# Kernel optimization log

Hardware: AMD Instinct MI355X
Metric: run time of the kernel (lower is better)

Reference implementation:

```python
import jax, jax.numpy as jnp
import numpy as np
from jax import lax

V, D = 100000, 300          # vocab, embedding dim (pretrained_embeds shape)
F, FS, K = 256, 3, 5        # nof_filters, filters_size, k_for_maxpool
B, NS, LS, LQ = 64, 50, 60, 32  # batch, n_sents per doc, sent len, question len


def setup_inputs() -> dict:
    key = jax.random.key(0)
    ks = jax.random.split(key, 8)
    sentences = jax.random.randint(ks[0], (B, NS, LS), 0, V)
    question = jax.random.randint(ks[1], (B, LQ), 0, V)
    target_sents = jax.random.randint(ks[2], (B, NS), 0, 2)
    target_docs = jax.random.randint(ks[3], (B,), 0, 2)
    embeds = jax.random.normal(ks[4], (V, D), dtype=jnp.float32)          # frozen pretrained table
    filters = jax.random.normal(ks[5], (F, 1, FS, D), dtype=jnp.float32)  # shared quest/sent conv filters
    W = jax.random.normal(ks[6], (6,), dtype=jnp.float32) * 0.4           # linear_per_q weight
    b = jax.random.normal(ks[7], (1,), dtype=jnp.float32) * 0.1           # linear_per_q bias
    return dict(sentences=sentences, question=question, target_sents=target_sents,
                target_docs=target_docs, embeds=embeds, filters=filters, W=W, b=b)


def _conv(x, filters):
    # x: [N,L,D], filters: [F,1,FS,D] -> [N,L,F]; matches F.conv2d(pad=(FS-1,0)) then slicing last L rows
    fs = filters.shape[2]
    L = x.shape[1]
    y = lax.conv_general_dilated(x[:, None, :, :], filters, (1, 1),
                                 ((fs - 1, fs - 1), (0, 0)),
                                 dimension_numbers=('NCHW', 'OIHW', 'NCHW'))  # [N,F,L+fs-1,1]
    return jnp.transpose(y[:, :, -L:, 0], (0, 2, 1))


def _cos(q, s):
    # q: [B,LQ,d], s: [B,NS,LS,d] -> [NS,B,LQ,LS] cosine similarity matrices
    num = jnp.einsum('bqd,bnld->nbql', q, s)
    qn = jnp.linalg.norm(q, axis=-1)                      # [B,LQ]
    sn = jnp.transpose(jnp.linalg.norm(s, axis=-1), (1, 0, 2))  # [NS,B,LS]
    return num / (qn[None, :, :, None] * sn[:, :, None, :])


def _pool(sim, k):
    # k-max pooling over the sentence-length axis -> stack [max, mean-of-top-k]
    top = lax.top_k(sim, k)[0]
    return jnp.stack([top[..., 0], jnp.mean(top, axis=-1)], axis=-1)


def _bce(p, t):
    eps = 1e-7
    p = jnp.clip(p, eps, 1.0 - eps)
    return -jnp.mean(t * jnp.log(p) + (1.0 - t) * jnp.log1p(-p))


def reference(sentences, question, target_sents, target_docs, embeds, filters, W, b):
    qe = embeds[question]                                 # [B,LQ,D]
    se = embeds[sentences]                                # [B,NS,LS,D]
    sim_ins = _cos(qe, se)                                # [NS,B,LQ,LS]
    sim_oh = (sim_ins >= 1.0 - 1e-5).astype(jnp.float32)  # exact-match channel (unmasked, as in original)
    qc = _conv(qe, filters)                               # [B,LQ,F]
    sc = _conv(se.reshape(B * NS, LS, D), filters).reshape(B, NS, LS, F)
    sim_sen = _cos(qc, sc)                                # [NS,B,LQ,LS]
    qmask = (question > 0).astype(jnp.float32)            # pad id = 0
    smask = (sentences > 0).astype(jnp.float32)
    m = qmask[None, :, :, None] * jnp.transpose(smask, (1, 0, 2))[:, :, None, :]
    feats = jnp.concatenate([_pool(sim_ins * m, K), _pool(sim_sen * m, K), _pool(sim_oh, K)], axis=-1)
    feats = jnp.transpose(feats, (1, 0, 2, 3))            # [B,NS,LQ,6]
    sent_out = jax.nn.sigmoid(feats @ W + b[0])           # [B,NS,LQ]
    sentence_relevance = jnp.mean(sent_out, axis=-1)      # [B,NS]
    document_emitions = jnp.max(sentence_relevance, axis=-1)  # [B]
    loss = (_bce(sentence_relevance, target_sents.astype(jnp.float32)) +
            _bce(document_emitions, target_docs.astype(jnp.float32))) / 2.0
    return loss, sentence_relevance, document_emitions
```

## Files before the change

### kernel.cpp

```cpp
#include <hip/hip_runtime.h>
#include <math.h>

#define VB  64
#define NSS 50
#define LSS 60
#define LQQ 32
#define DD  300
#define FF  256

#define SEST 312
#define SROWS 66
#define SCST 264
#define SIMST 66
#define KKC 29
#define KKI 10
#define KKS 8

typedef __attribute__((ext_vector_type(8))) short bfrag;
typedef __attribute__((ext_vector_type(4))) float ffrag;

__device__ __forceinline__ unsigned short f2bf(float v) {
    unsigned int x = __float_as_uint(v);
    x += 0x7fffu + ((x >> 16) & 1u);
    return (unsigned short)(x >> 16);
}
__device__ __forceinline__ float bf2f(unsigned short u) {
    return __uint_as_float(((unsigned int)u) << 16);
}

__global__ __launch_bounds__(256) void k_fprep(const float* __restrict__ filters,
                                               unsigned short* __restrict__ filt_frag) {
    int idx0 = (blockIdx.x * 256 + threadIdx.x) * 4;
    int j0 = idx0 & 7, ln = (idx0 >> 3) & 63, nt = (idx0 >> 9) & 15, kk = idx0 >> 13;
    int f = nt * 16 + (ln & 15);
    int k0 = kk * 32 + ((ln >> 4) << 3) + j0;
    int t = k0 / SEST, d0 = k0 - t * SEST;
    ushort4 h = {0, 0, 0, 0};
    if (t < 3 && d0 < DD) {
        float4 v = *(const float4*)(filters + f * 900 + t * DD + d0);
        h.x = f2bf(v.x); h.y = f2bf(v.y); h.z = f2bf(v.z); h.w = f2bf(v.w);
    }
    *(ushort4*)(filt_frag + idx0) = h;
}

__global__ __launch_bounds__(512) void k_qprep(const int* __restrict__ question,
                                               const float* __restrict__ embeds,
                                               const unsigned short* __restrict__ filt_frag,
                                               unsigned short* __restrict__ qe_frag,
                                               unsigned short* __restrict__ qc_frag,
                                               float* __restrict__ q_inv,
                                               float* __restrict__ qc_inv) {
    const int b = blockIdx.x, tid = threadIdx.x, lane = tid & 63, w = tid >> 6;
    const int quad = lane >> 4, m16 = lane & 15;
    __shared__ __align__(16) unsigned short qeb[34 * SEST];
    __shared__ __align__(16) unsigned short qcb[LQQ * SCST];
    const int* qrow = question + b * LQQ;
    {
        ushort4 z4 = {0, 0, 0, 0};
        for (int i = tid; i < 96; i += 512) {
            int r = i / 3, c = 300 + (i - r * 3) * 4;
            *(ushort4*)(qeb + r * SEST + c) = z4;
        }
        for (int i = tid; i < 156; i += 512) {
            int r = i / 78, c = (i - r * 78) * 4;
            *(ushort4*)(qeb + (LQQ + r) * SEST + c) = z4;
        }
    }
    for (int i = tid; i < LQQ * 75; i += 512) {
        int r = i / 75, c = (i - r * 75) * 4;
        float4 v = *(const float4*)(embeds + (size_t)qrow[r] * DD + c);
        ushort4 h;
        h.x = f2bf(v.x); h.y = f2bf(v.y); h.z = f2bf(v.z); h.w = f2bf(v.w);
        *(ushort4*)(qeb + r * SEST + c) = h;
    }
    __syncthreads();
    if (tid < 256) {
        int r = tid >> 3, part = tid & 7;
        float s = 0.f;
        #pragma unroll
        for (int it = 0; it < 5; ++it) {
            if (!(it == 4 && part == 7)) {
                int c = part * 8 + it * 64;
                uint4 u = *(const uint4*)(qeb + r * SEST + c);
                float a0 = bf2f((unsigned short)(u.x & 0xffff)), a1 = bf2f((unsigned short)(u.x >> 16));
                float a2 = bf2f((unsigned short)(u.y & 0xffff)), a3 = bf2f((unsigned short)(u.y >> 16));
                float a4 = bf2f((unsigned short)(u.z & 0xffff)), a5 = bf2f((unsigned short)(u.z >> 16));
                float a6 = bf2f((unsigned short)(u.w & 0xffff)), a7 = bf2f((unsigned short)(u.w >> 16));
                s += a0 * a0 + a1 * a1 + a2 * a2 + a3 * a3 + a4 * a4 + a5 * a5 + a6 * a6 + a7 * a7;
            }
        }
        s += __shfl_down(s, 4, 64);
        s += __shfl_down(s, 2, 64);
        s += __shfl_down(s, 1, 64);
        if (part == 0) q_inv[b * LQQ + r] = 1.f / sqrtf(s);
    }
    for (int i8 = tid; i8 < KKI * 2 * 64; i8 += 512) {
        int ln = i8 & 63, mt = (i8 >> 6) & 1, kk = i8 >> 7;
        int q = mt * 16 + (ln & 15);
        int k0 = kk * 32 + ((ln >> 4) << 3);
        uint4 v = {0, 0, 0, 0};
        if (k0 < SEST) v = *(const uint4*)(qeb + q * SEST + k0);
        *(uint4*)(qe_frag + (size_t)b * (KKI * 2 * 512) + (size_t)i8 * 8) = v;
    }
    const int mtq = w & 1, w4 = (w >> 1) * 4;
    ffrag acc[4];
    #pragma unroll
    for (int i = 0; i < 4; ++i) acc[i] = (ffrag)0.f;
    {
        const bfrag* fF = (const bfrag*)filt_frag;
        bfrag bb[4], nb[4];
        #pragma unroll
        for (int i = 0; i < 4; ++i) bb[i] = fF[(w4 + i) * 64 + lane];
        for (int kk = 0; kk < KKC; ++kk) {
            if (kk + 1 < KKC) {
                #pragma unroll
                for (int i = 0; i < 4; ++i) nb[i] = fF[((kk + 1) * 16 + w4 + i) * 64 + lane];
            }
            const int kb = kk * 32 + quad * 8;
            bfrag a0 = *(const bfrag*)(qeb + (mtq * 16 + m16) * SEST + kb);
            #pragma unroll
            for (int i = 0; i < 4; ++i)
                acc[i] = __builtin_amdgcn_mfma_f32_16x16x32_bf16(a0, bb[i], acc[i], 0, 0, 0);
            #pragma unroll
            for (int i = 0; i < 4; ++i) bb[i] = nb[i];
        }
    }
    #pragma unroll
    for (int i = 0; i < 4; ++i) {
        int f = (w4 + i) * 16 + m16;
        #pragma unroll
        for (int r = 0; r < 4; ++r) {
            int q = mtq * 16 + quad * 4 + r;
            qcb[q * SCST + f] = f2bf(acc[i][r]);
        }
    }
    __syncthreads();
    if (tid < 256) {
        int r = tid >> 3, part = tid & 7;
        float s = 0.f;
        #pragma unroll
        for (int it = 0; it < 4; ++it) {
            int c = part * 8 + it * 64;
            uint4 u = *(const uint4*)(qcb + r * SCST + c);
            float a0 = bf2f((unsigned short)(u.x & 0xffff)), a1 = bf2f((unsigned short)(u.x >> 16));
            float a2 = bf2f((unsigned short)(u.y & 0xffff)), a3 = bf2f((unsigned short)(u.y >> 16));
            float a4 = bf2f((unsigned short)(u.z & 0xffff)), a5 = bf2f((unsigned short)(u.z >> 16));
            float a6 = bf2f((unsigned short)(u.w & 0xffff)), a7 = bf2f((unsigned short)(u.w >> 16));
            s += a0 * a0 + a1 * a1 + a2 * a2 + a3 * a3 + a4 * a4 + a5 * a5 + a6 * a6 + a7 * a7;
        }
        s += __shfl_down(s, 4, 64);
        s += __shfl_down(s, 2, 64);
        s += __shfl_down(s, 1, 64);
        if (part == 0) qc_inv[b * LQQ + r] = 1.f / sqrtf(s);
    }
    for (int i8 = tid; i8 < KKS * 2 * 64; i8 += 512) {
        int ln = i8 & 63, mt = (i8 >> 6) & 1, kk = i8 >> 7;
        int q = mt * 16 + (ln & 15);
        int k0 = kk * 32 + ((ln >> 4) << 3);
        *(uint4*)(qc_frag + (size_t)b * (KKS * 2 * 512) + (size_t)i8 * 8) =
            *(const uint4*)(qcb + q * SCST + k0);
    }
}

#define CONV_STEP(KKV, BB0, BB1) do {                                              \
    const int kb_ = (KKV) * 32 + quad * 8;                                         \
    bfrag a0_ = *(const bfrag*)(seb + (m16) * SEST + kb_);                         \
    bfrag a1_ = *(const bfrag*)(seb + (16 + m16) * SEST + kb_);                    \
    bfrag a2_ = *(const bfrag*)(seb + (32 + m16) * SEST + kb_);                    \
    bfrag a3_ = *(const bfrag*)(seb + (48 + m16) * SEST + kb_);                    \
    __builtin_amdgcn_s_setprio(1);                                                 \
    acc[0][0] = __builtin_amdgcn_mfma_f32_16x16x32_bf16(a0_, BB0, acc[0][0], 0, 0, 0); \
    acc[0][1] = __builtin_amdgcn_mfma_f32_16x16x32_bf16(a0_, BB1, acc[0][1], 0, 0, 0); \
    acc[1][0] = __builtin_amdgcn_mfma_f32_16x16x32_bf16(a1_, BB0, acc[1][0], 0, 0, 0); \
    acc[1][1] = __builtin_amdgcn_mfma_f32_16x16x32_bf16(a1_, BB1, acc[1][1], 0, 0, 0); \
    acc[2][0] = __builtin_amdgcn_mfma_f32_16x16x32_bf16(a2_, BB0, acc[2][0], 0, 0, 0); \
    acc[2][1] = __builtin_amdgcn_mfma_f32_16x16x32_bf16(a2_, BB1, acc[2][1], 0, 0, 0); \
    acc[3][0] = __builtin_amdgcn_mfma_f32_16x16x32_bf16(a3_, BB0, acc[3][0], 0, 0, 0); \
    acc[3][1] = __builtin_amdgcn_mfma_f32_16x16x32_bf16(a3_, BB1, acc[3][1], 0, 0, 0); \
    __builtin_amdgcn_s_setprio(0);                                                 \
} while (0)

__global__ __launch_bounds__(512, 6) void k_sent(
    const int* __restrict__ sentences, const int* __restrict__ question,
    const float* __restrict__ embeds,
    const unsigned short* __restrict__ filt_frag,
    const unsigned short* __restrict__ qe_frag,
    const unsigned short* __restrict__ qc_frag,
    const float* __restrict__ q_inv, const float* __restrict__ qc_inv,
    const float* __restrict__ W6, const float* __restrict__ b1,
    float* __restrict__ d_out) {
    const int blk = blockIdx.x;
    const int b = blk / NSS, n = blk - b * NSS;
    const int tid = threadIdx.x, lane = tid & 63, w = tid >> 6;
    const int quad = lane >> 4, m16 = lane & 15;
    const int w2 = w * 2;

    __shared__ __align__(16) unsigned short seb[SROWS * SEST];
    __shared__ __align__(16) float sim[LQQ * SIMST];
    __shared__ float sinv[64], scninv[64];
    __shared__ int sid[64];
    __shared__ int qid[LQQ];
    __shared__ float qm[LQQ], qiv[LQQ], qciv[LQQ];
    __shared__ float featq[LQQ][4];
    __shared__ float pr[LQQ];
    unsigned short* scb = seb;

    const bfrag* fF = (const bfrag*)filt_frag;
    bfrag b0a = fF[(w2) * 64 + lane];
    bfrag b0b = fF[(w2 + 1) * 64 + lane];

    const int* srow = sentences + ((size_t)b * NSS + n) * LSS;
    if (tid < 64) sid[tid] = (tid < LSS) ? srow[tid] : 0;
    if (tid < LQQ) {
        int qi = question[b * LQQ + tid];
        qid[tid] = qi; qm[tid] = qi > 0 ? 1.f : 0.f;
        qiv[tid] = q_inv[b * LQQ + tid]; qciv[tid] = qc_inv[b * LQQ + tid];
    }
    {
        ushort4 z4 = {0, 0, 0, 0};
        for (int i = tid; i < 180; i += 512) {
            int r = i / 3, c = 300 + (i - r * 3) * 4;
            *(ushort4*)(seb + r * SEST + c) = z4;
        }
        for (int i = tid; i < 468; i += 512) {
            int r = i / 78, c = (i - r * 78) * 4;
            *(ushort4*)(seb + (60 + r) * SEST + c) = z4;
        }
    }
    for (int i = tid; i < LSS * 75; i += 512) {
        int r = i / 75, c = (i - r * 75) * 4;
        float4 v = *(const float4*)(embeds + (size_t)srow[r] * DD + c);
        ushort4 h;
        h.x = f2bf(v.x); h.y = f2bf(v.y); h.z = f2bf(v.z); h.w = f2bf(v.w);
        *(ushort4*)(seb + r * SEST + c) = h;
    }
    __syncthreads();
    if (tid < 480) {
        int r = tid >> 3, part = tid & 7;
        float s = 0.f;
        #pragma unroll
        for (int it = 0; it < 5; ++it) {
            if (!(it == 4 && part == 7)) {
                int c = part * 8 + it * 64;
                uint4 u = *(const uint4*)(seb + r * SEST + c);
                float a0 = bf2f((unsigned short)(u.x & 0xffff)), a1 = bf2f((unsigned short)(u.x >> 16));
                float a2 = bf2f((unsigned short)(u.y & 0xffff)), a3 = bf2f((unsigned short)(u.y >> 16));
                float a4 = bf2f((unsigned short)(u.z & 0xffff)), a5 = bf2f((unsigned short)(u.z >> 16));
                float a6 = bf2f((unsigned short)(u.w & 0xffff)), a7 = bf2f((unsigned short)(u.w >> 16));
                s += a0 * a0 + a1 * a1 + a2 * a2 + a3 * a3 + a4 * a4 + a5 * a5 + a6 * a6 + a7 * a7;
            }
        }
        s += __shfl_down(s, 4, 64);
        s += __shfl_down(s, 2, 64);
        s += __shfl_down(s, 1, 64);
        if (part == 0) sinv[r] = 1.f / sqrtf(s);
    }
    if (tid >= 480 && tid < 484) sinv[60 + tid - 480] = 0.f;
    __syncthreads();

    ffrag acc[4][2];
    #pragma unroll
    for (int mt = 0; mt < 4; ++mt)
        #pragma unroll
        for (int i = 0; i < 2; ++i) acc[mt][i] = (ffrag)0.f;
    {
        bfrag b1a, b1b;
        for (int kk = 0; kk + 2 <= KKC; kk += 2) {
            b1a = fF[((kk + 1) * 16 + w2) * 64 + lane];
            b1b = fF[((kk + 1) * 16 + w2 + 1) * 64 + lane];
            CONV_STEP(kk, b0a, b0b);
            if (kk + 2 < KKC) {
                b0a = fF[((kk + 2) * 16 + w2) * 64 + lane];
                b0b = fF[((kk + 2) * 16 + w2 + 1) * 64 + lane];
            }
            CONV_STEP(kk + 1, b1a, b1b);
        }
        CONV_STEP(KKC - 1, b0a, b0b);
    }
    {
        const int mt = w >> 2, nt = w & 3;
        const bfrag* qF = (const bfrag*)qe_frag + ((size_t)b * KKI * 2 + mt) * 64 + lane;
        const unsigned short* sebr = seb + (nt * 16 + m16) * SEST + quad * 8;
        ffrag c0 = (ffrag)0.f;
        bfrag aq0 = qF[0];
        for (int kk = 0; kk < KKI; kk += 2) {
            bfrag aq1 = qF[(kk + 1) * 128];
            bfrag bL0 = *(const bfrag*)(sebr + kk * 32);
            c0 = __builtin_amdgcn_mfma_f32_16x16x32_bf16(aq0, bL0, c0, 0, 0, 0);
            if (kk + 2 < KKI) aq0 = qF[(kk + 2) * 128];
            bfrag bL1 = *(const bfrag*)(sebr + (kk + 1) * 32);
            c0 = __builtin_amdgcn_mfma_f32_16x16x32_bf16(aq1, bL1, c0, 0, 0, 0);
        }
        const int l_ = nt * 16 + m16;
        const float sm = sinv[l_] * (sid[l_] > 0 ? 1.f : 0.f);
        #pragma unroll
        for (int r = 0; r < 4; ++r) {
            int q = mt * 16 + quad * 4 + r;
            sim[q * SIMST + l_] = c0[r] * (qiv[q] * qm[q]) * sm;
        }
    }
    __syncthreads();

    if (tid < 256) {
        ushort4 z4 = {0, 0, 0, 0};
        int r4 = 60 + (tid >> 6), c4 = (tid & 63) * 4;
        *(ushort4*)(scb + r4 * SCST + c4) = z4;
    }
    #pragma unroll
    for (int mt = 0; mt < 4; ++mt)
        #pragma unroll
        for (int i = 0; i < 2; ++i) {
            int f = (w2 + i) * 16 + m16;
            #pragma unroll
            for (int r = 0; r < 4; ++r) {
                int l = mt * 16 + quad * 4 + r;
                scb[l * SCST + f] = f2bf(acc[mt][i][r]);
            }
        }
    if (tid < LQQ) {
        int q = tid;
        float t0 = -1e30f, t1 = -1e30f, t2 = -1e30f, t3 = -1e30f, t4 = -1e30f;
        for (int l = 0; l < LSS; ++l) {
            float v = sim[q * SIMST + l];
            if (v > t4) {
                if (v > t0)      { t4 = t3; t3 = t2; t2 = t1; t1 = t0; t0 = v; }
                else if (v > t1) { t4 = t3; t3 = t2; t2 = t1; t1 = v; }
                else if (v > t2) { t4 = t3; t3 = t2; t2 = v; }
                else if (v > t3) { t4 = t3; t3 = v; }
                else               t4 = v;
            }
        }
        featq[q][0] = t0;
        featq[q][1] = (t0 + t1 + t2 + t3 + t4) * 0.2f;
        int qi = qid[q], c = 0;
        for (int l = 0; l < LSS; ++l) c += (sid[l] == qi) ? 1 : 0;
        featq[q][2] = c > 0 ? 1.f : 0.f;
        featq[q][3] = (float)(c < 5 ? c : 5) * 0.2f;
    }
    __syncthreads();
    if (tid < 480) {
        int r = tid >> 3, part = tid & 7;
        float s = 0.f;
        #pragma unroll
        for (int it = 0; it < 4; ++it) {
            int c = part * 8 + it * 64;
            uint4 u = *(const uint4*)(scb + r * SCST + c);
            float a0 = bf2f((unsigned short)(u.x & 0xffff)), a1 = bf2f((unsigned short)(u.x >> 16));
            float a2 = bf2f((unsigned short)(u.y & 0xffff)), a3 = bf2f((unsigned short)(u.y >> 16));
            float a4 = bf2f((unsigned short)(u.z & 0xffff)), a5 = bf2f((unsigned short)(u.z >> 16));
            float a6 = bf2f((unsigned short)(u.w & 0xffff)), a7 = bf2f((unsigned short)(u.w >> 16));
            s += a0 * a0 + a1 * a1 + a2 * a2 + a3 * a3 + a4 * a4 + a5 * a5 + a6 * a6 + a7 * a7;
        }
        s += __shfl_down(s, 4, 64);
        s += __shfl_down(s, 2, 64);
        s += __shfl_down(s, 1, 64);
        if (part == 0) scninv[r] = 1.f / sqrtf(s);
    }
    if (tid >= 480 && tid < 484) scninv[60 + tid - 480] = 0.f;
    __syncthreads();
    {
        const int mt = w >> 2, nt = w & 3;
        const bfrag* qF = (const bfrag*)qc_frag + ((size_t)b * KKS * 2 + mt) * 64 + lane;
        const unsigned short* scbr = scb + (nt * 16 + m16) * SCST + quad * 8;
        ffrag c0 = (ffrag)0.f;
        bfrag aq0 = qF[0];
        for (int kk = 0; kk < KKS; kk += 2) {
            bfrag aq1 = qF[(kk + 1) * 128];
            bfrag bL0 = *(const bfrag*)(scbr + kk * 32);
            c0 = __builtin_amdgcn_mfma_f32_16x16x32_bf16(aq0, bL0, c0, 0, 0, 0);
            if (kk + 2 < KKS) aq0 = qF[(kk + 2) * 128];
            bfrag bL1 = *(const bfrag*)(scbr + (kk + 1) * 32);
            c0 = __builtin_amdgcn_mfma_f32_16x16x32_bf16(aq1, bL1, c0, 0, 0, 0);
        }
        const int l_ = nt * 16 + m16;
        const float sm = scninv[l_] * (sid[l_] > 0 ? 1.f : 0.f);
        #pragma unroll
        for (int r = 0; r < 4; ++r) {
            int q = mt * 16 + quad * 4 + r;
            sim[q * SIMST + l_] = c0[r] * (qciv[q] * qm[q]) * sm;
        }
    }
    __syncthreads();
    if (tid < LQQ) {
        int q = tid;
        float t0 = -1e30f, t1 = -1e30f, t2 = -1e30f, t3 = -1e30f, t4 = -1e30f;
        for (int l = 0; l < LSS; ++l) {
            float v = sim[q * SIMST + l];
            if (v > t4) {
                if (v > t0)      { t4 = t3; t3 = t2; t2 = t1; t1 = t0; t0 = v; }
                else if (v > t1) { t4 = t3; t3 = t2; t2 = t1; t1 = v; }
                else if (v > t2) { t4 = t3; t3 = t2; t2 = v; }
                else if (v > t3) { t4 = t3; t3 = v; }
                else               t4 = v;
            }
        }
        float smax = t0, smean = (t0 + t1 + t2 + t3 + t4) * 0.2f;
        float z = featq[q][0] * W6[0] + featq[q][1] * W6[1] + smax * W6[2] + smean * W6[3]
                + featq[q][2] * W6[4] + featq[q][3] * W6[5] + b1[0];
        pr[q] = 1.f / (1.f + expf(-z));
    }
    __syncthreads();
    if (w == 0) {
        float s = (lane < LQQ) ? pr[lane] : 0.f;
        s += __shfl_down(s, 16, 64);
        s += __shfl_down(s, 8, 64);
        s += __shfl_down(s, 4, 64);
        s += __shfl_down(s, 2, 64);
        s += __shfl_down(s, 1, 64);
        if (lane == 0) d_out[1 + (size_t)b * NSS + n] = s * (1.f / 32.f);
    }
}

__global__ __launch_bounds__(256) void k_final(const int* __restrict__ tsent,
                                               const int* __restrict__ tdoc,
                                               float* __restrict__ d_out) {
    const int tid = threadIdx.x;
    __shared__ float sh[256];
    __shared__ float docs[VB];
    if (tid < VB) {
        float m = -1e30f;
        for (int nn = 0; nn < NSS; ++nn) m = fmaxf(m, d_out[1 + tid * NSS + nn]);
        docs[tid] = m;
        d_out[1 + VB * NSS + tid] = m;
    }
    float s = 0.f;
    for (int i = tid; i < VB * NSS; i += 256) {
        float p = d_out[1 + i];
        p = fminf(fmaxf(p, 1e-7f), 1.f - 1e-7f);
        float t = (float)tsent[i];
        s += t * logf(p) + (1.f - t) * log1pf(-p);
    }
    sh[tid] = s;
    __syncthreads();
    for (int st = 128; st > 0; st >>= 1) {
        if (tid < st) sh[tid] += sh[tid + st];
        __syncthreads();
    }
    float ls = 0.f;
    if (tid == 0) ls = -sh[0] / (float)(VB * NSS);
    __syncthreads();
    float s2 = 0.f;
    if (tid < VB) {
        float p = fminf(fmaxf(docs[tid], 1e-7f), 1.f - 1e-7f);
        float t = (float)tdoc[tid];
        s2 = t * logf(p) + (1.f - t) * log1pf(-p);
    }
    sh[tid] = s2;
    __syncthreads();
    for (int st = 128; st > 0; st >>= 1) {
        if (tid < st) sh[tid] += sh[tid + st];
        __syncthreads();
    }
    if (tid == 0) {
        float ld = -sh[0] / (float)VB;
        d_out[0] = 0.5f * (ls + ld);
    }
}

extern "C" void kernel_launch(void* const* d_in, const int* in_sizes, int n_in,
                              void* d_out, int out_size, void* d_ws, size_t ws_size,
                              hipStream_t stream) {
    const int*   sentences = (const int*)d_in[0];
    const int*   question  = (const int*)d_in[1];
    const int*   tsent     = (const int*)d_in[2];
    const int*   tdoc      = (const int*)d_in[3];
    const float* embeds    = (const float*)d_in[4];
    const float* filters   = (const float*)d_in[5];
    const float* W6        = (const float*)d_in[6];
    const float* b1        = (const float*)d_in[7];
    float* out = (float*)d_out;

    float* ws = (float*)d_ws;
    float* q_inv  = ws;
    float* qc_inv = ws + 2048;
    unsigned short* qe_frag  = (unsigned short*)(ws + 4096);
    unsigned short* qc_frag  = qe_frag + 655360;
    unsigned short* filt_frag = qc_frag + 524288;

    k_fprep<<<232, 256, 0, stream>>>(filters, filt_frag);
    k_qprep<<<VB, 512, 0, stream>>>(question, embeds, filt_frag, qe_frag, qc_frag, q_inv, qc_inv);
    k_sent<<<VB * NSS, 512, 0, stream>>>(sentences, question, embeds,
                                         filt_frag, qe_frag, qc_frag,
                                         q_inv, qc_inv, W6, b1, out);
    k_final<<<1, 256, 0, stream>>>(tsent, tdoc, out);
}
```

Before: 398.9 us.

## Fuse sentence norms into embedding gather and conv norms into MFMA epilogue

Squared norms of the sentence embeddings are now accumulated in fp32 while the rows are gathered and converted to bf16, instead of in a separate pass that re-reads shared memory. Conv-output norms are reduced straight from the MFMA accumulators with cross-lane shuffles into a small per-warp partial table, which removes another shared-memory pass. The question features stay in registers, so two block-wide barriers and a shared-memory round trip go away. Norms are now taken from fp32 values rather than bf16-rounded ones, which shifts the numerics slightly. Padded rows can produce inf*0, but they lie outside the range the top-k reads.

```diff
diff --git a/kernel.cpp b/kernel.cpp
--- a/kernel.cpp
+++ b/kernel.cpp
@@ -197,12 +197,11 @@
 
     __shared__ __align__(16) unsigned short seb[SROWS * SEST];
     __shared__ __align__(16) float sim[LQQ * SIMST];
-    __shared__ float sinv[64], scninv[64];
+    __shared__ float sinv[64];
+    __shared__ float pnorm[64][8];
     __shared__ int sid[64];
     __shared__ int qid[LQQ];
     __shared__ float qm[LQQ], qiv[LQQ], qciv[LQQ];
-    __shared__ float featq[LQQ][4];
-    __shared__ float pr[LQQ];
     unsigned short* scb = seb;
 
     const bfrag* fF = (const bfrag*)filt_frag;
@@ -227,35 +226,26 @@
             *(ushort4*)(seb + (60 + r) * SEST + c) = z4;
         }
     }
-    for (int i = tid; i < LSS * 75; i += 512) {
-        int r = i / 75, c = (i - r * 75) * 4;
-        float4 v = *(const float4*)(embeds + (size_t)srow[r] * DD + c);
-        ushort4 h;
-        h.x = f2bf(v.x); h.y = f2bf(v.y); h.z = f2bf(v.z); h.w = f2bf(v.w);
-        *(ushort4*)(seb + r * SEST + c) = h;
-    }
-    __syncthreads();
-    if (tid < 480) {
-        int r = tid >> 3, part = tid & 7;
-        float s = 0.f;
-        #pragma unroll
-        for (int it = 0; it < 5; ++it) {
-            if (!(it == 4 && part == 7)) {
-                int c = part * 8 + it * 64;
-                uint4 u = *(const uint4*)(seb + r * SEST + c);
-                float a0 = bf2f((unsigned short)(u.x & 0xffff)), a1 = bf2f((unsigned short)(u.x >> 16));
-                float a2 = bf2f((unsigned short)(u.y & 0xffff)), a3 = bf2f((unsigned short)(u.y >> 16));
-                float a4 = bf2f((unsigned short)(u.z & 0xffff)), a5 = bf2f((unsigned short)(u.z >> 16));
-                float a6 = bf2f((unsigned short)(u.w & 0xffff)), a7 = bf2f((unsigned short)(u.w >> 16));
-                s += a0 * a0 + a1 * a1 + a2 * a2 + a3 * a3 + a4 * a4 + a5 * a5 + a6 * a6 + a7 * a7;
-            }
-        }
-        s += __shfl_down(s, 4, 64);
-        s += __shfl_down(s, 2, 64);
-        s += __shfl_down(s, 1, 64);
-        if (part == 0) sinv[r] = 1.f / sqrtf(s);
-    }
-    if (tid >= 480 && tid < 484) sinv[60 + tid - 480] = 0.f;
+    {
+        const int g = tid >> 3, part = tid & 7;
+        if (g < LSS) {
+            const float* erow = embeds + (size_t)srow[g] * DD;
+            float s = 0.f;
+            for (int c = part * 4; c < DD; c += 32) {
+                float4 v = *(const float4*)(erow + c);
+                s += v.x * v.x + v.y * v.y + v.z * v.z + v.w * v.w;
+                ushort4 h;
+                h.x = f2bf(v.x); h.y = f2bf(v.y); h.z = f2bf(v.z); h.w = f2bf(v.w);
+                *(ushort4*)(seb + g * SEST + c) = h;
+            }
+            s += __shfl_down(s, 4, 8);
+            s += __shfl_down(s, 2, 8);
+            s += __shfl_down(s, 1, 8);
+            if (part == 0) sinv[g] = 1.f / sqrtf(s);
+        } else if (part == 0) {
+            sinv[g] = 0.f;
+        }
+    }
     __syncthreads();
 
     ffrag acc[4][2];
@@ -301,11 +291,7 @@
     }
     __syncthreads();
 
-    if (tid < 256) {
-        ushort4 z4 = {0, 0, 0, 0};
-        int r4 = 60 + (tid >> 6), c4 = (tid & 63) * 4;
-        *(ushort4*)(scb + r4 * SCST + c4) = z4;
-    }
+    float fq0 = 0.f, fq1 = 0.f, fq2 = 0.f, fq3 = 0.f;
     #pragma unroll
     for (int mt = 0; mt < 4; ++mt)
         #pragma unroll
@@ -316,6 +302,17 @@
                 int l = mt * 16 + quad * 4 + r;
                 scb[l * SCST + f] = f2bf(acc[mt][i][r]);
             }
+        }
+    #pragma unroll
+    for (int mt = 0; mt < 4; ++mt)
+        #pragma unroll
+        for (int r = 0; r < 4; ++r) {
+            float s = acc[mt][0][r] * acc[mt][0][r] + acc[mt][1][r] * acc[mt][1][r];
+            s += __shfl_down(s, 8, 16);
+            s += __shfl_down(s, 4, 16);
+            s += __shfl_down(s, 2, 16);
+            s += __shfl_down(s, 1, 16);
+            if (m16 == 0) pnorm[mt * 16 + quad * 4 + r][w] = s;
         }
     if (tid < LQQ) {
         int q = tid;
@@ -330,34 +327,15 @@
                 else               t4 = v;
             }
         }
-        featq[q][0] = t0;
-        featq[q][1] = (t0 + t1 + t2 + t3 + t4) * 0.2f;
+        fq0 = t0;
+        fq1 = (t0 + t1 + t2 + t3 + t4) * 0.2f;
         int qi = qid[q], c = 0;
         for (int l = 0; l < LSS; ++l) c += (sid[l] == qi) ? 1 : 0;
-        featq[q][2] = c > 0 ? 1.f : 0.f;
-        featq[q][3] = (float)(c < 5 ? c : 5) * 0.2f;
-    }
-    __syncthreads();
-    if (tid < 480) {
-        int r = tid >> 3, part = tid & 7;
-        float s = 0.f;
-        #pragma unroll
-        for (int it = 0; it < 4; ++it) {
-            int c = part * 8 + it * 64;
-            uint4 u = *(const uint4*)(scb + r * SCST + c);
-            float a0 = bf2f((unsigned short)(u.x & 0xffff)), a1 = bf2f((unsigned short)(u.x >> 16));
-            float a2 = bf2f((unsigned short)(u.y & 0xffff)), a3 = bf2f((unsigned short)(u.y >> 16));
-            float a4 = bf2f((unsigned short)(u.z & 0xffff)), a5 = bf2f((unsigned short)(u.z >> 16));
-            float a6 = bf2f((unsigned short)(u.w & 0xffff)), a7 = bf2f((unsigned short)(u.w >> 16));
-            s += a0 * a0 + a1 * a1 + a2 * a2 + a3 * a3 + a4 * a4 + a5 * a5 + a6 * a6 + a7 * a7;
-        }
-        s += __shfl_down(s, 4, 64);
-        s += __shfl_down(s, 2, 64);
-        s += __shfl_down(s, 1, 64);
-        if (part == 0) scninv[r] = 1.f / sqrtf(s);
-    }
-    if (tid >= 480 && tid < 484) scninv[60 + tid - 480] = 0.f;
-    __syncthreads();
+        fq2 = c > 0 ? 1.f : 0.f;
+        fq3 = (float)(c < 5 ? c : 5) * 0.2f;
+    }
+    __syncthreads();
+
     {
         const int mt = w >> 2, nt = w & 3;
         const bfrag* qF = (const bfrag*)qc_frag + ((size_t)b * KKS * 2 + mt) * 64 + lane;
@@ -373,7 +351,10 @@
             c0 = __builtin_amdgcn_mfma_f32_16x16x32_bf16(aq1, bL1, c0, 0, 0, 0);
         }
         const int l_ = nt * 16 + m16;
-        const float sm = scninv[l_] * (sid[l_] > 0 ? 1.f : 0.f);
+        float ssum = 0.f;
+        #pragma unroll
+        for (int t = 0; t < 8; ++t) ssum += pnorm[l_][t];
+        const float sm = (1.f / sqrtf(ssum)) * (sid[l_] > 0 ? 1.f : 0.f);
         #pragma unroll
         for (int r = 0; r < 4; ++r) {
             int q = mt * 16 + quad * 4 + r;
@@ -381,33 +362,33 @@
         }
     }
     __syncthreads();
-    if (tid < LQQ) {
-        int q = tid;
-        float t0 = -1e30f, t1 = -1e30f, t2 = -1e30f, t3 = -1e30f, t4 = -1e30f;
-        for (int l = 0; l < LSS; ++l) {
-            float v = sim[q * SIMST + l];
-            if (v > t4) {
-                if (v > t0)      { t4 = t3; t3 = t2; t2 = t1; t1 = t0; t0 = v; }
-                else if (v > t1) { t4 = t3; t3 = t2; t2 = t1; t1 = v; }
-                else if (v > t2) { t4 = t3; t3 = t2; t2 = v; }
-                else if (v > t3) { t4 = t3; t3 = v; }
-                else               t4 = v;
-            }
-        }
-        float smax = t0, smean = (t0 + t1 + t2 + t3 + t4) * 0.2f;
-        float z = featq[q][0] * W6[0] + featq[q][1] * W6[1] + smax * W6[2] + smean * W6[3]
-                + featq[q][2] * W6[4] + featq[q][3] * W6[5] + b1[0];
-        pr[q] = 1.f / (1.f + expf(-z));
-    }
-    __syncthreads();
+
     if (w == 0) {
-        float s = (lane < LQQ) ? pr[lane] : 0.f;
-        s += __shfl_down(s, 16, 64);
-        s += __shfl_down(s, 8, 64);
-        s += __shfl_down(s, 4, 64);
-        s += __shfl_down(s, 2, 64);
-        s += __shfl_down(s, 1, 64);
-        if (lane == 0) d_out[1 + (size_t)b * NSS + n] = s * (1.f / 32.f);
+        float prv = 0.f;
+        if (lane < LQQ) {
+            int q = lane;
+            float t0 = -1e30f, t1 = -1e30f, t2 = -1e30f, t3 = -1e30f, t4 = -1e30f;
+            for (int l = 0; l < LSS; ++l) {
+                float v = sim[q * SIMST + l];
+                if (v > t4) {
+                    if (v > t0)      { t4 = t3; t3 = t2; t2 = t1; t1 = t0; t0 = v; }
+                    else if (v > t1) { t4 = t3; t3 = t2; t2 = t1; t1 = v; }
+                    else if (v > t2) { t4 = t3; t3 = t2; t2 = v; }
+                    else if (v > t3) { t4 = t3; t3 = v; }
+                    else               t4 = v;
+                }
+            }
+            float smax = t0, smean = (t0 + t1 + t2 + t3 + t4) * 0.2f;
+            float z = fq0 * W6[0] + fq1 * W6[1] + smax * W6[2] + smean * W6[3]
+                    + fq2 * W6[4] + fq3 * W6[5] + b1[0];
+            prv = 1.f / (1.f + expf(-z));
+        }
+        prv += __shfl_down(prv, 16, 64);
+        prv += __shfl_down(prv, 8, 64);
+        prv += __shfl_down(prv, 4, 64);
+        prv += __shfl_down(prv, 2, 64);
+        prv += __shfl_down(prv, 1, 64);
+        if (lane == 0) d_out[1 + (size_t)b * NSS + n] = prv * (1.f / 32.f);
     }
 }
 
```

New measurement: 410.2 us. 2.8% more time.
